# Kernel tuning notes

Hardware: AMD Instinct MI355X
Metric: run time of the kernel (lower is better)

Reference implementation:

```python
import jax, jax.numpy as jnp
import numpy as np

B, S, D = 2, 11253, 256
NHEAD, NLEVEL, DFF = 8, 4, 1024
KERNEL = 2
NPOINT = KERNEL * KERNEL
HEAD_DIM = D // NHEAD
LEVEL_SHAPES = [(92, 92), (46, 46), (23, 23), (12, 12)]
LEVEL_STARTS = np.cumsum([0] + [h * w for h, w in LEVEL_SHAPES])[:-1]


def _kernel_indices():
    # BoxeR _create_kernel_indices: even kernel -> [-0.5, 0.5]/K, (x, y) order
    idx = np.arange(KERNEL, dtype=np.float32) - (KERNEL - 1) / 2.0
    i, j = np.meshgrid(idx, idx, indexing="ij")
    return jnp.asarray(np.stack([j, i], -1).reshape(-1, 2) / KERNEL)


KIDX = _kernel_indices()  # (NPOINT, 2) box-relative sample offsets


def layer_norm(x, w, b, eps=1e-5):
    mu = x.mean(-1, keepdims=True)
    var = ((x - mu) ** 2).mean(-1, keepdims=True)
    return (x - mu) * jax.lax.rsqrt(var + eps) * w + b


def setup_inputs() -> dict:
    key = jax.random.key(0)
    ks = jax.random.split(key, 12)

    def p(i, shape, scale=0.02):
        return jax.random.normal(ks[i], shape, jnp.float32) * scale

    cxcy = jax.random.uniform(ks[2], (B, S, 2), jnp.float32, minval=0.1, maxval=0.9)
    wh = jax.random.uniform(ks[3], (B, S, 2), jnp.float32, minval=0.02, maxval=0.2)
    return dict(
        src=jax.random.normal(ks[0], (B, S, D), jnp.float32),
        pos=jax.random.normal(ks[1], (B, S, D), jnp.float32),
        src_shape=jnp.asarray(np.array(LEVEL_SHAPES, np.int32)),
        src_mask=jnp.zeros((B, S), jnp.bool_),
        src_start_index=jnp.asarray(LEVEL_STARTS.astype(np.int32)),
        src_valid_ratios=jnp.ones((B, NLEVEL, 2), jnp.float32),
        ref_windows=jnp.concatenate([cxcy, wh], -1),
        value_w=p(4, (D, D)), value_b=jnp.zeros((D,), jnp.float32),
        out_w=p(5, (D, D)), out_b=jnp.zeros((D,), jnp.float32),
        box_w=p(6, (NHEAD * NLEVEL * 4, D)), box_b=jnp.zeros((NHEAD * NLEVEL * 4,), jnp.float32),
        attn_w=p(7, (NHEAD * NLEVEL * NPOINT, D)), attn_b=jnp.zeros((NHEAD * NLEVEL * NPOINT,), jnp.float32),
        lin1_w=p(8, (DFF, D)), lin1_b=jnp.zeros((DFF,), jnp.float32),
        lin2_w=p(9, (D, DFF)), lin2_b=jnp.zeros((D,), jnp.float32),
        norm1_w=jnp.ones((D,), jnp.float32), norm1_b=jnp.zeros((D,), jnp.float32),
        norm2_w=jnp.ones((D,), jnp.float32), norm2_b=jnp.zeros((D,), jnp.float32),
    )


def box_attention(q, src, src_mask, src_valid_ratios, ref_windows,
                  value_w, value_b, out_w, out_b, box_w, box_b, attn_w, attn_b):
    value = src @ value_w.T + value_b
    value = jnp.where(src_mask[..., None], 0.0, value)
    value = value.reshape(B, S, NHEAD, HEAD_DIM)

    # where-to-attend: per-head, per-level box offsets decoded around ref_windows (cx,cy,w,h)
    off = (q @ box_w.T + box_b).reshape(B, S, NHEAD, NLEVEL, 4)
    ref = ref_windows[:, :, None, None, :]
    boxes = ref + off / 8.0 * ref[..., jnp.array([2, 3, 2, 3])]
    center, size = boxes[..., None, :2], boxes[..., None, 2:]
    grid = center + KIDX * jax.nn.relu(size)  # (B,S,nh,L,P,2) in normalized [0,1] coords
    grid = grid * src_valid_ratios[:, None, None, :, None, :]

    attn = (q @ attn_w.T + attn_b).reshape(B, S, NHEAD, NLEVEL * NPOINT)
    attn = jax.nn.softmax(attn, -1).reshape(B, S, NHEAD, NLEVEL, NPOINT)

    out = jnp.zeros((B, NHEAD, S, HEAD_DIM), src.dtype)
    for lvl, (H, W) in enumerate(LEVEL_SHAPES):
        s0 = int(LEVEL_STARTS[lvl])
        v = jnp.transpose(value[:, s0:s0 + H * W], (0, 2, 1, 3))  # (B,nh,HW,hd)
        loc = jnp.transpose(grid[:, :, :, lvl], (0, 2, 1, 3, 4))  # (B,nh,S,P,2)
        # grid_sample bilinear, align_corners=False, zero padding
        px = loc[..., 0] * W - 0.5
        py = loc[..., 1] * H - 0.5
        x0, y0 = jnp.floor(px), jnp.floor(py)
        wx, wy = (px - x0)[..., None], (py - y0)[..., None]

        def gather(ix, iy):
            valid = (ix >= 0) & (ix < W) & (iy >= 0) & (iy < H)
            idx = (jnp.clip(iy, 0, H - 1) * W + jnp.clip(ix, 0, W - 1)).astype(jnp.int32)
            g = jnp.take_along_axis(v, idx.reshape(B, NHEAD, S * NPOINT)[..., None], axis=2)
            return g.reshape(B, NHEAD, S, NPOINT, HEAD_DIM) * valid[..., None]

        g00, g01 = gather(x0, y0), gather(x0 + 1, y0)
        g10, g11 = gather(x0, y0 + 1), gather(x0 + 1, y0 + 1)
        samp = (g00 * (1 - wx) + g01 * wx) * (1 - wy) + (g10 * (1 - wx) + g11 * wx) * wy
        aw = jnp.transpose(attn[:, :, :, lvl], (0, 2, 1, 3))  # (B,nh,S,P)
        out = out + jnp.einsum("bhspd,bhsp->bhsd", samp, aw)

    out = jnp.transpose(out, (0, 2, 1, 3)).reshape(B, S, D)
    return out @ out_w.T + out_b


def reference(src, pos, src_shape, src_mask, src_start_index, src_valid_ratios,
              ref_windows, value_w, value_b, out_w, out_b, box_w, box_b,
              attn_w, attn_b, lin1_w, lin1_b, lin2_w, lin2_b,
              norm1_w, norm1_b, norm2_w, norm2_b):
    # self-attn (box attention) + residual + LN
    src2 = box_attention(src + pos, src, src_mask, src_valid_ratios, ref_windows,
                         value_w, value_b, out_w, out_b, box_w, box_b, attn_w, attn_b)
    x = layer_norm(src + src2, norm1_w, norm1_b)
    # FFN + residual + LN (dropout=0 in eval)
    ff = jax.nn.relu(x @ lin1_w.T + lin1_b) @ lin2_w.T + lin2_b
    return layer_norm(x + ff, norm2_w, norm2_b)
```

## Files before the change

kernel.cpp:

```cpp
#include <hip/hip_runtime.h>
#include <hip/hip_bf16.h>
#include <hip/hip_fp16.h>

#define TOKENS 22506
#define SLEN   11253

typedef __bf16 bf16x8 __attribute__((ext_vector_type(8)));
typedef float  f32x4  __attribute__((ext_vector_type(4)));
typedef float  f32x2  __attribute__((ext_vector_type(2)));
typedef uint   u32x4  __attribute__((ext_vector_type(4)));
typedef uint   u32x2  __attribute__((ext_vector_type(2)));

#if defined(__has_builtin)
#if __has_builtin(__builtin_amdgcn_cvt_pk_f32_fp8) && __has_builtin(__builtin_amdgcn_cvt_pk_fp8_f32)
#define HAS_FP8CVT 1
#endif
#endif

__device__ __forceinline__ ushort f2bu(float f) {
    __hip_bfloat16 h = __float2bfloat16(f);
    return *reinterpret_cast<ushort*>(&h);
}
__device__ __forceinline__ float bu2f(ushort u) {
    return __uint_as_float((uint)u << 16);
}
__device__ __forceinline__ uint pkf16(float a, float b) {
    __half2 h = __floats2half2_rn(a, b);
    return *reinterpret_cast<uint*>(&h);
}
__device__ __forceinline__ void gl16(const void* g, void* l) {
    __builtin_amdgcn_global_load_lds(
        (__attribute__((address_space(1))) void*)(g),
        (__attribute__((address_space(3))) void*)(l), 16, 0, 0);
}

#ifndef HAS_FP8CVT
__device__ __forceinline__ uint enc_fp8(float x) {
    if (!(fabsf(x) >= 0.f)) return 0;
    uint u = __float_as_uint(x);
    uint s = (u >> 24) & 0x80u;
    float ax = fabsf(x);
    if (ax >= 448.f) return s | 0x7Eu;
    if (ax < 0.0009765625f) return s;
    int e; frexpf(ax, &e);
    int ue = e - 1;
    if (ue < -6) {
        int m = (int)(ax * 512.f + 0.5f);
        if (m > 7) m = 7;
        return s | (uint)m;
    }
    float q = ax * exp2f((float)(3 - ue));
    int mi = (int)(q + 0.5f);
    if (mi >= 16) { mi >>= 1; ++ue; if (ue > 8) return s | 0x7Eu; }
    return s | ((uint)(ue + 7) << 3) | ((uint)mi & 7u);
}
__device__ __forceinline__ float dec_fp8(uint b) {
    const float sgn = (b & 0x80u) ? -1.f : 1.f;
    const uint e = (b >> 3) & 15u, m = b & 7u;
    if (e == 0) return sgn * (float)m * 0.001953125f;
    return sgn * (1.0f + (float)m * 0.125f) * exp2f((float)e - 7.f);
}
#endif

__device__ __forceinline__ uint fp8pack4(float f0, float f1, float f2, float f3) {
#ifdef HAS_FP8CVT
    int p = 0;
    p = __builtin_amdgcn_cvt_pk_fp8_f32(f0, f1, p, false);
    p = __builtin_amdgcn_cvt_pk_fp8_f32(f2, f3, p, true);
    return (uint)p;
#else
    return enc_fp8(f0) | (enc_fp8(f1) << 8) | (enc_fp8(f2) << 16) | (enc_fp8(f3) << 24);
#endif
}
__device__ __forceinline__ uint fp8pack1(float f) {
#ifdef HAS_FP8CVT
    return (uint)__builtin_amdgcn_cvt_pk_fp8_f32(f, f, 0, false) & 0xFFu;
#else
    return enc_fp8(f);
#endif
}
template<bool HI>
__device__ __forceinline__ f32x2 fp8pair(uint w) {
#ifdef HAS_FP8CVT
    auto c = __builtin_amdgcn_cvt_pk_f32_fp8((int)w, HI);
    f32x2 r; r.x = c[0]; r.y = c[1]; return r;
#else
    const uint sh = HI ? 16u : 0u;
    f32x2 r; r.x = dec_fp8((w >> sh) & 0xFFu); r.y = dec_fp8((w >> (sh + 8)) & 0xFFu);
    return r;
#endif
}

__device__ __forceinline__ void xcd_swz(int& bx, int& by) {
    const int nx = gridDim.x, ny = gridDim.y;
    if ((nx & 7) == 0) {
        const int L = blockIdx.x + nx * blockIdx.y;
        const int chunk = nx >> 3;
        const int k = L & 7, j = L >> 3;
        bx = k * chunk + (j % chunk);
        by = j / chunk;
        if (by >= ny) { bx = blockIdx.x; by = blockIdx.y; }
    } else {
        bx = blockIdx.x; by = blockIdx.y;
    }
}

template<bool RELU, bool NTSTORE, bool F8Z0>
__global__ __launch_bounds__(256) void gemm_small(
    const ushort* __restrict__ A0, const ushort* __restrict__ W0,
    const float* __restrict__ b0, void* __restrict__ C0,
    const ushort* __restrict__ A1, const ushort* __restrict__ W1,
    const float* __restrict__ b1, void* __restrict__ C1,
    int M, int N, int K)
{
    const bool zz = blockIdx.z != 0;
    const ushort* A   = zz ? A1 : A0;
    const ushort* W   = zz ? W1 : W0;
    const float* bias = zz ? b1 : b0;
    void* Cptr        = zz ? C1 : C0;

    __shared__ ushort smem[12288];
    const int tid  = threadIdx.x;
    const int lane = tid & 63;
    const int wid  = tid >> 6;
    const int wr = wid >> 1, wc = wid & 1;
    int bx, by; xcd_swz(bx, by);
    const int m0 = bx * 64, n0 = by * 128;
    const int lrow = lane & 15, lhi = lane >> 4;

    const int arow = tid >> 2;
    const int scol = (tid & 3) << 3;
    const ushort* ga  = A + (size_t)min(m0 + arow, M - 1) * K + scol;
    const ushort* gb0 = W + (size_t)(n0 + arow)      * K + scol;
    const ushort* gb1 = W + (size_t)(n0 + arow + 64) * K + scol;

    f32x4 acc[2][4] = {};
    const int NT = K >> 5;

    gl16(ga,  &smem[tid * 8]);
    gl16(gb0, &smem[4096 + tid * 8]);
    gl16(gb1, &smem[4096 + tid * 8 + 2048]);

    int cur = 0;
    for (int t = 0; t < NT; ++t) {
        __syncthreads();
        if (t + 1 < NT) {
            const int k0 = (t + 1) << 5;
            const int nb = cur ^ 1;
            gl16(ga  + k0, &smem[nb * 2048 + tid * 8]);
            gl16(gb0 + k0, &smem[4096 + nb * 4096 + tid * 8]);
            gl16(gb1 + k0, &smem[4096 + nb * 4096 + tid * 8 + 2048]);
        }
        bf16x8 afr[2], bfr[4];
        #pragma unroll
        for (int m = 0; m < 2; ++m)
            afr[m] = *reinterpret_cast<const bf16x8*>(
                &smem[cur * 2048 + (wr * 32 + m * 16 + lrow) * 32 + lhi * 8]);
        #pragma unroll
        for (int n = 0; n < 4; ++n)
            bfr[n] = *reinterpret_cast<const bf16x8*>(
                &smem[4096 + cur * 4096 + (wc * 64 + n * 16 + lrow) * 32 + lhi * 8]);
        #pragma unroll
        for (int m = 0; m < 2; ++m)
            #pragma unroll
            for (int n = 0; n < 4; ++n)
                acc[m][n] = __builtin_amdgcn_mfma_f32_16x16x32_bf16(
                    afr[m], bfr[n], acc[m][n], 0, 0, 0);
        cur ^= 1;
    }

    __syncthreads();
    #pragma unroll
    for (int m = 0; m < 2; ++m) {
        #pragma unroll
        for (int n = 0; n < 4; ++n) {
            const int col = wc * 64 + n * 16 + lrow;
            const float bv = bias[n0 + col];
            #pragma unroll
            for (int r = 0; r < 4; ++r) {
                const int row = wr * 32 + m * 16 + lhi * 4 + r;
                float v = acc[m][n][r] + bv;
                if (RELU) v = fmaxf(v, 0.f);
                smem[row * 136 + col] = f2bu(v);
            }
        }
    }
    __syncthreads();
    if (F8Z0 && !zz) {
        #pragma unroll
        for (int i = 0; i < 4; ++i) {
            const int e = tid + i * 256;
            const int row = e >> 4, ch = e & 15;
            if (m0 + row < M) {
                const u32x4 v = *reinterpret_cast<const u32x4*>(&smem[row * 136 + ch * 8]);
                float f[8];
                #pragma unroll
                for (int j = 0; j < 4; ++j) {
                    f[2 * j]     = __uint_as_float(v[j] << 16);
                    f[2 * j + 1] = __uint_as_float(v[j] & 0xFFFF0000u);
                }
                u32x2 o;
                o[0] = fp8pack4(f[0], f[1], f[2], f[3]);
                o[1] = fp8pack4(f[4], f[5], f[6], f[7]);
                u32x2* dst = reinterpret_cast<u32x2*>(
                    (unsigned char*)Cptr + (size_t)(m0 + row) * N + n0 + ch * 8);
                if (NTSTORE) __builtin_nontemporal_store(o, dst);
                else *dst = o;
            }
        }
    } else {
        #pragma unroll
        for (int i = 0; i < 4; ++i) {
            const int e = tid + i * 256;
            const int row = e >> 4, ch = e & 15;
            if (m0 + row < M) {
                const u32x4 v = *reinterpret_cast<const u32x4*>(&smem[row * 136 + ch * 8]);
                u32x4* dst = reinterpret_cast<u32x4*>(
                    (ushort*)Cptr + (size_t)(m0 + row) * N + n0 + ch * 8);
                if (NTSTORE) __builtin_nontemporal_store(v, dst);
                else *dst = v;
            }
        }
    }
}

__global__ __launch_bounds__(256) void gemm_f8(
    const unsigned char* __restrict__ A, const unsigned char* __restrict__ W,
    const float* __restrict__ bias, ushort* __restrict__ C,
    int M, int N, int K)
{
    __shared__ unsigned char smem[17408];
    const int tid  = threadIdx.x;
    const int lane = tid & 63;
    const int wid  = tid >> 6;
    const int wr = wid >> 1, wc = wid & 1;
    int bx, by; xcd_swz(bx, by);
    const int m0 = bx * 64, n0 = by * 128;
    const int lrow = lane & 15, lhi = lane >> 4;

    const int arow = tid >> 1;
    const int achk = (tid & 1) << 4;
    const unsigned char* ga = A + (size_t)min(m0 + (arow & 63), M - 1) * K + achk;
    const unsigned char* gb = W + (size_t)(n0 + arow) * K + achk;

    f32x4 acc[2][4] = {};
    const int NT = K >> 5;

    if (tid < 128) gl16(ga, &smem[tid * 16]);
    gl16(gb, &smem[4096 + tid * 16]);

    int cur = 0;
    for (int t = 0; t < NT; ++t) {
        __syncthreads();
        if (t + 1 < NT) {
            const int k0 = (t + 1) << 5;
            const int nb = cur ^ 1;
            if (tid < 128) gl16(ga + k0, &smem[nb * 2048 + tid * 16]);
            gl16(gb + k0, &smem[4096 + nb * 4096 + tid * 16]);
        }
        long afr[2], bfr[4];
        #pragma unroll
        for (int m = 0; m < 2; ++m)
            afr[m] = *reinterpret_cast<const long*>(
                &smem[cur * 2048 + (wr * 32 + m * 16 + lrow) * 32 + lhi * 8]);
        #pragma unroll
        for (int n = 0; n < 4; ++n)
            bfr[n] = *reinterpret_cast<const long*>(
                &smem[4096 + cur * 4096 + (wc * 64 + n * 16 + lrow) * 32 + lhi * 8]);
        #pragma unroll
        for (int m = 0; m < 2; ++m)
            #pragma unroll
            for (int n = 0; n < 4; ++n)
                acc[m][n] = __builtin_amdgcn_mfma_f32_16x16x32_fp8_fp8(
                    afr[m], bfr[n], acc[m][n], 0, 0, 0);
        cur ^= 1;
    }

    __syncthreads();
    ushort* sm16 = reinterpret_cast<ushort*>(smem);
    #pragma unroll
    for (int m = 0; m < 2; ++m) {
        #pragma unroll
        for (int n = 0; n < 4; ++n) {
            const int col = wc * 64 + n * 16 + lrow;
            const float bv = bias[n0 + col];
            #pragma unroll
            for (int r = 0; r < 4; ++r) {
                const int row = wr * 32 + m * 16 + lhi * 4 + r;
                sm16[row * 136 + col] = f2bu(acc[m][n][r] + bv);
            }
        }
    }
    __syncthreads();
    #pragma unroll
    for (int i = 0; i < 4; ++i) {
        const int e = tid + i * 256;
        const int row = e >> 4, ch = e & 15;
        if (m0 + row < M) {
            const u32x4 v = *reinterpret_cast<const u32x4*>(&sm16[row * 136 + ch * 8]);
            *reinterpret_cast<u32x4*>(C + (size_t)(m0 + row) * N + n0 + ch * 8) = v;
        }
    }
}

__global__ __launch_bounds__(256) void prep_all(
    const float* __restrict__ vw, const float* __restrict__ bw,
    const float* __restrict__ aw, const float* __restrict__ ow,
    const float* __restrict__ l1, const float* __restrict__ l2,
    const float* __restrict__ bb, const float* __restrict__ ab,
    ushort* __restrict__ dstW, float* __restrict__ dstQB,
    unsigned char* __restrict__ dstW8,
    const float4* __restrict__ src, const float4* __restrict__ pos,
    ushort4* __restrict__ srcb, ushort4* __restrict__ qb)
{
    const int blk = blockIdx.x;
    if (blk < 2817) {
        const int i = blk * 256 + threadIdx.x;
        if (i < 720896) {
            float v;
            if      (i <  65536) v = vw[i];
            else if (i <  98304) v = bw[i -  65536];
            else if (i < 131072) v = aw[i -  98304];
            else if (i < 196608) v = ow[i - 131072];
            else if (i < 458752) v = l1[i - 196608];
            else                 v = l2[i - 458752];
            dstW[i] = f2bu(v);
            if (i >= 458752) dstW8[i - 458752] = (unsigned char)fp8pack1(v);
        } else if (i < 721152) {
            const int j = i - 720896;
            dstQB[j] = (j < 128) ? bb[j] : ab[j - 128];
        }
    } else {
        const int i = (blk - 2817) * 256 + threadIdx.x;
        if (i >= TOKENS * 64) return;
        const float4 s = src[i], p = pos[i];
        ushort4 us, uq;
        us.x = f2bu(s.x); us.y = f2bu(s.y); us.z = f2bu(s.z); us.w = f2bu(s.w);
        uq.x = f2bu(s.x + p.x); uq.y = f2bu(s.y + p.y);
        uq.z = f2bu(s.z + p.z); uq.w = f2bu(s.w + p.w);
        srcb[i] = us; qb[i] = uq;
    }
}

__global__ __launch_bounds__(256) void box_fused(
    const unsigned char* __restrict__ val,
    const ushort* __restrict__ qout,
    const float* __restrict__ refw,
    const float* __restrict__ vratio,
    ushort* __restrict__ attnout)
{
    __shared__ ushort4 offs[64 * 17];
    __shared__ uint2 wts[64 * 17];
    const int tid = threadIdx.x;

    int work;
    {
        const int x = blockIdx.x & 7, s = blockIdx.x >> 3;
        work = (x < 4) ? (s * 4 + x) : (1408 + s * 4 + (x - 4));
        if ((int)gridDim.x != 2814 || work >= (int)gridDim.x) work = blockIdx.x;
    }
    const int t0 = work * 8;

    {
        const int u = tid >> 2, lvl = tid & 3;
        const int t = min(t0 + (u >> 3), TOKENS - 1);
        const int h = u & 7;
        const int b = (t >= SLEN) ? 1 : 0;
        const ushort* qr = qout + (size_t)t * 256;

        const uint2 lu = *reinterpret_cast<const uint2*>(qr + 128 + h * 16 + lvl * 4);
        float e0 = __uint_as_float(lu.x << 16);
        float e1 = __uint_as_float(lu.x & 0xFFFF0000u);
        float e2 = __uint_as_float(lu.y << 16);
        float e3 = __uint_as_float(lu.y & 0xFFFF0000u);
        float mx = fmaxf(fmaxf(e0, e1), fmaxf(e2, e3));
        mx = fmaxf(mx, __shfl_xor(mx, 1));
        mx = fmaxf(mx, __shfl_xor(mx, 2));
        e0 = __expf(e0 - mx); e1 = __expf(e1 - mx);
        e2 = __expf(e2 - mx); e3 = __expf(e3 - mx);
        float ss = e0 + e1 + e2 + e3;
        ss += __shfl_xor(ss, 1);
        ss += __shfl_xor(ss, 2);
        const float inv = 1.f / ss;
        const float pe[4] = { e0 * inv, e1 * inv, e2 * inv, e3 * inv };

        const uint2 ou = *reinterpret_cast<const uint2*>(qr + h * 16 + lvl * 4);
        const float o0 = __uint_as_float(ou.x << 16) * 0.125f;
        const float o1 = __uint_as_float(ou.x & 0xFFFF0000u) * 0.125f;
        const float o2 = __uint_as_float(ou.y << 16) * 0.125f;
        const float o3 = __uint_as_float(ou.y & 0xFFFF0000u) * 0.125f;

        const float4 rw = *reinterpret_cast<const float4*>(refw + (size_t)t * 4);
        const int Ww = (lvl == 0) ? 92 : (lvl == 1) ? 46 : (lvl == 2) ? 23 : 12;
        const int s0 = (lvl == 0) ? 0 : (lvl == 1) ? 8464 : (lvl == 2) ? 10580 : 11109;
        const float vrx = vratio[(b * 4 + lvl) * 2 + 0];
        const float vry = vratio[(b * 4 + lvl) * 2 + 1];

        const float bx  = rw.x + o0 * rw.z;
        const float by  = rw.y + o1 * rw.w;
        const float bwd = fmaxf(rw.z + o2 * rw.z, 0.f);
        const float bhd = fmaxf(rw.w + o3 * rw.w, 0.f);

        #pragma unroll
        for (int k = 0; k < 4; ++k) {
            const float jx = (k & 1) ? 0.25f : -0.25f;
            const float iy = (k & 2) ? 0.25f : -0.25f;
            const float px = (bx + jx * bwd) * vrx * (float)Ww - 0.5f;
            const float py = (by + iy * bhd) * vry * (float)Ww - 0.5f;
            const float x0f = floorf(px), y0f = floorf(py);
            const int x0 = (int)x0f, y0 = (int)y0f;
            const float wx = px - x0f, wy = py - y0f;
            const float wp = pe[k];

            const bool vx0 = (x0 >= 0) && (x0 < Ww);
            const bool vx1 = (x0 + 1 >= 0) && (x0 + 1 < Ww);
            const bool vy0 = (y0 >= 0) && (y0 < Ww);
            const bool vy1 = (y0 + 1 >= 0) && (y0 + 1 < Ww);
            const int cx0 = min(max(x0, 0), Ww - 1);
            const int cx1 = min(max(x0 + 1, 0), Ww - 1);
            const int cy0 = min(max(y0, 0), Ww - 1);
            const int cy1 = min(max(y0 + 1, 0), Ww - 1);

            const float w00 = (vx0 && vy0) ? wp * (1.f - wx) * (1.f - wy) : 0.f;
            const float w01 = (vx1 && vy0) ? wp * wx         * (1.f - wy) : 0.f;
            const float w10 = (vx0 && vy1) ? wp * (1.f - wx) * wy         : 0.f;
            const float w11 = (vx1 && vy1) ? wp * wx         * wy         : 0.f;

            ushort4 sp;
            sp.x = (ushort)(s0 + cy0 * Ww + cx0);
            sp.y = (ushort)(s0 + cy0 * Ww + cx1);
            sp.z = (ushort)(s0 + cy1 * Ww + cx0);
            sp.w = (ushort)(s0 + cy1 * Ww + cx1);

            const int p = lvl * 4 + k;
            offs[u * 17 + p] = sp;
            wts[u * 17 + p]  = make_uint2(pkf16(w00, w01), pkf16(w10, w11));
        }
    }
    __syncthreads();

    const int u = tid >> 2, dl = tid & 3;
    const int traw = t0 + (u >> 3);
    const int t = min(traw, TOKENS - 1);
    const int h = u & 7;
    const uint boff = ((t >= SLEN) ? (uint)SLEN * 256u : 0u) + (uint)h * 32u + (uint)dl * 8u;
    const char* base = (const char*)val;

    const ushort4* po = &offs[u * 17];
    const uint2* pw = &wts[u * 17];
    f32x2 a0 = {0.f, 0.f}, a1 = {0.f, 0.f}, a2 = {0.f, 0.f}, a3 = {0.f, 0.f};

    uint2 vA[16], vB[16];

    auto issue = [&](int g, uint2 (&v)[16]) {
        #pragma unroll
        for (int q = 0; q < 4; ++q) {
            const ushort4 sp = po[g * 4 + q];
            v[q * 4 + 0] = *reinterpret_cast<const uint2*>(base + (((uint)sp.x << 8) + boff));
            v[q * 4 + 1] = *reinterpret_cast<const uint2*>(base + (((uint)sp.y << 8) + boff));
            v[q * 4 + 2] = *reinterpret_cast<const uint2*>(base + (((uint)sp.z << 8) + boff));
            v[q * 4 + 3] = *reinterpret_cast<const uint2*>(base + (((uint)sp.w << 8) + boff));
        }
    };
    auto consume = [&](int g, uint2 (&v)[16]) {
        #pragma unroll
        for (int q = 0; q < 4; ++q) {
            const uint2 w2 = pw[g * 4 + q];
            const float2 wl = __half22float2(*reinterpret_cast<const __half2*>(&w2.x));
            const float2 wh = __half22float2(*reinterpret_cast<const __half2*>(&w2.y));
            const float wq[4] = { wl.x, wl.y, wh.x, wh.y };
            #pragma unroll
            for (int c = 0; c < 4; ++c) {
                const uint2 vv = v[q * 4 + c];
                f32x2 wv; wv.x = wq[c]; wv.y = wq[c];
                a0 += wv * fp8pair<false>(vv.x);
                a1 += wv * fp8pair<true>(vv.x);
                a2 += wv * fp8pair<false>(vv.y);
                a3 += wv * fp8pair<true>(vv.y);
            }
        }
    };

    issue(0, vA);
    issue(1, vB);
    __builtin_amdgcn_sched_barrier(0);
    consume(0, vA);
    issue(2, vA);
    __builtin_amdgcn_sched_barrier(0);
    consume(1, vB);
    issue(3, vB);
    __builtin_amdgcn_sched_barrier(0);
    consume(2, vA);
    consume(3, vB);

    if (traw < TOKENS) {
        u32x4 o;
        o[0] = (uint)f2bu(a0.x) | ((uint)f2bu(a0.y) << 16);
        o[1] = (uint)f2bu(a1.x) | ((uint)f2bu(a1.y) << 16);
        o[2] = (uint)f2bu(a2.x) | ((uint)f2bu(a2.y) << 16);
        o[3] = (uint)f2bu(a3.x) | ((uint)f2bu(a3.y) << 16);
        *reinterpret_cast<u32x4*>(attnout + (size_t)t * 256 + h * 32 + dl * 8) = o;
    }
}

template<bool AF32, bool OUTF32>
__global__ __launch_bounds__(256) void ln_add2(
    const void* __restrict__ aptr, const ushort* __restrict__ bptr,
    const float* __restrict__ w, const float* __restrict__ bias,
    void* __restrict__ outp, int nrows)
{
    const int lane = threadIdx.x & 63, wv = threadIdx.x >> 6;
    const int row = blockIdx.x * 4 + wv;
    if (row >= nrows) return;
    const size_t base = (size_t)row * 256 + lane * 4;

    float4 av;
    if (AF32) {
        av = *reinterpret_cast<const float4*>((const float*)aptr + base);
    } else {
        const ushort4 u = *reinterpret_cast<const ushort4*>((const ushort*)aptr + base);
        av = make_float4(bu2f(u.x), bu2f(u.y), bu2f(u.z), bu2f(u.w));
    }
    const ushort4 ub = *reinterpret_cast<const ushort4*>(bptr + base);
    const float v0 = av.x + bu2f(ub.x), v1 = av.y + bu2f(ub.y);
    const float v2 = av.z + bu2f(ub.z), v3 = av.w + bu2f(ub.w);

    float s = v0 + v1 + v2 + v3;
    #pragma unroll
    for (int o = 32; o; o >>= 1) s += __shfl_xor(s, o);
    const float mu = s * (1.f / 256.f);
    const float d0 = v0 - mu, d1 = v1 - mu, d2 = v2 - mu, d3 = v3 - mu;
    float s2 = d0 * d0 + d1 * d1 + d2 * d2 + d3 * d3;
    #pragma unroll
    for (int o = 32; o; o >>= 1) s2 += __shfl_xor(s2, o);
    const float rs = rsqrtf(s2 * (1.f / 256.f) + 1e-5f);

    const float4 w4 = *reinterpret_cast<const float4*>(w + lane * 4);
    const float4 g4 = *reinterpret_cast<const float4*>(bias + lane * 4);
    const float r0 = d0 * rs * w4.x + g4.x;
    const float r1 = d1 * rs * w4.y + g4.y;
    const float r2 = d2 * rs * w4.z + g4.z;
    const float r3 = d3 * rs * w4.w + g4.w;
    if (OUTF32) {
        *reinterpret_cast<float4*>((float*)outp + base) = make_float4(r0, r1, r2, r3);
    } else {
        ushort4 u;
        u.x = f2bu(r0); u.y = f2bu(r1); u.z = f2bu(r2); u.w = f2bu(r3);
        *reinterpret_cast<ushort4*>((ushort*)outp + base) = u;
    }
}

extern "C" void kernel_launch(void* const* d_in, const int* in_sizes, int n_in,
                              void* d_out, int out_size, void* d_ws, size_t ws_size,
                              hipStream_t stream)
{
    const float* src     = (const float*)d_in[0];
    const float* pos     = (const float*)d_in[1];
    const float* vratio  = (const float*)d_in[5];
    const float* refw    = (const float*)d_in[6];
    const float* value_w = (const float*)d_in[7];
    const float* value_b = (const float*)d_in[8];
    const float* out_w   = (const float*)d_in[9];
    const float* out_b   = (const float*)d_in[10];
    const float* box_w   = (const float*)d_in[11];
    const float* box_b   = (const float*)d_in[12];
    const float* attn_w  = (const float*)d_in[13];
    const float* attn_b  = (const float*)d_in[14];
    const float* lin1_w  = (const float*)d_in[15];
    const float* lin1_b  = (const float*)d_in[16];
    const float* lin2_w  = (const float*)d_in[17];
    const float* lin2_b  = (const float*)d_in[18];
    const float* n1w     = (const float*)d_in[19];
    const float* n1b     = (const float*)d_in[20];
    const float* n2w     = (const float*)d_in[21];
    const float* n2b     = (const float*)d_in[22];

    char* wsb = (char*)d_ws;
    ushort* Wb    = (ushort*)(wsb);
    float*  qcb   = (float*)(wsb + 1441792);
    ushort* srcb  = (ushort*)(wsb + 1442816);
    ushort* qb    = (ushort*)(wsb + 12965888);
    unsigned char* valb = (unsigned char*)(wsb + 24488960);
    ushort* qoutb = (ushort*)(wsb + 36012032);
    ushort* attb  = (ushort*)(wsb + 47535104);
    ushort* src2b = (ushort*)(wsb + 59058176);
    ushort* xbb   = (ushort*)(wsb + 70581248);
    unsigned char* hb8 = (unsigned char*)(wsb + 82104320);
    ushort* yb    = (ushort*)(wsb + 105150464);
    unsigned char* Wf8 = (unsigned char*)(wsb + 116673536);

    const dim3 blk(256);

    prep_all<<<dim3(8444), blk, 0, stream>>>(
        value_w, box_w, attn_w, out_w, lin1_w, lin2_w, box_b, attn_b, Wb, qcb,
        Wf8, (const float4*)src, (const float4*)pos, (ushort4*)srcb, (ushort4*)qb);

    gemm_small<false, false, true><<<dim3(352, 2, 2), blk, 0, stream>>>(
        srcb, Wb, value_b, valb,
        qb, Wb + 65536, qcb, qoutb, TOKENS, 256, 256);

    box_fused<<<dim3((TOKENS + 7) / 8), blk, 0, stream>>>(
        valb, qoutb, refw, vratio, attb);

    gemm_small<false, false, false><<<dim3(352, 2, 1), blk, 0, stream>>>(
        attb, Wb + 131072, out_b, src2b,
        attb, Wb + 131072, out_b, src2b, TOKENS, 256, 256);
    ln_add2<false, false><<<dim3((TOKENS + 3) / 4), blk, 0, stream>>>(
        srcb, src2b, n1w, n1b, xbb, TOKENS);
    gemm_small<true, true, true><<<dim3(352, 8, 1), blk, 0, stream>>>(
        xbb, Wb + 196608, lin1_b, hb8,
        xbb, Wb + 196608, lin1_b, hb8, TOKENS, 1024, 256);
    gemm_f8<<<dim3(352, 2), blk, 0, stream>>>(
        hb8, Wf8, lin2_b, yb, TOKENS, 256, 1024);
    ln_add2<false, true><<<dim3((TOKENS + 3) / 4), blk, 0, stream>>>(
        xbb, yb, n2w, n2b, (float*)d_out, TOKENS);
}
```

Before: 131.0 us.

## Split bilinear corners across lane pairs with 16-byte gathers and shuffle reduction

Changes the thread-to-work mapping in the deformable sampling kernel. Each lane now loads 16 fp8 channels per corner with 128-bit loads, covering only two of the four bilinear corners, instead of 8 channels for all four corners. The partial sums from the two corner groups are combined with an xor-shuffle before writing bf16 output. This halves the number of gather instructions in exchange for wider loads, more accumulator registers, and extra shuffles. It also drops the explicit double-buffered issue/consume schedule.

```diff
diff --git a/kernel.cpp b/kernel.cpp
--- a/kernel.cpp
+++ b/kernel.cpp
@@ -440,66 +440,79 @@
     __syncthreads();
 
     const int u = tid >> 2, dl = tid & 3;
+    const int hd = dl & 1;
+    const int cp = dl >> 1;
     const int traw = t0 + (u >> 3);
     const int t = min(traw, TOKENS - 1);
     const int h = u & 7;
-    const uint boff = ((t >= SLEN) ? (uint)SLEN * 256u : 0u) + (uint)h * 32u + (uint)dl * 8u;
+    const uint boff = ((t >= SLEN) ? (uint)SLEN * 256u : 0u)
+                    + (uint)h * 32u + (uint)hd * 16u;
     const char* base = (const char*)val;
 
     const ushort4* po = &offs[u * 17];
     const uint2* pw = &wts[u * 17];
-    f32x2 a0 = {0.f, 0.f}, a1 = {0.f, 0.f}, a2 = {0.f, 0.f}, a3 = {0.f, 0.f};
-
-    uint2 vA[16], vB[16];
-
-    auto issue = [&](int g, uint2 (&v)[16]) {
-        #pragma unroll
-        for (int q = 0; q < 4; ++q) {
-            const ushort4 sp = po[g * 4 + q];
-            v[q * 4 + 0] = *reinterpret_cast<const uint2*>(base + (((uint)sp.x << 8) + boff));
-            v[q * 4 + 1] = *reinterpret_cast<const uint2*>(base + (((uint)sp.y << 8) + boff));
-            v[q * 4 + 2] = *reinterpret_cast<const uint2*>(base + (((uint)sp.z << 8) + boff));
-            v[q * 4 + 3] = *reinterpret_cast<const uint2*>(base + (((uint)sp.w << 8) + boff));
-        }
+    f32x2 ac0 = {0,0}, ac1 = {0,0}, ac2 = {0,0}, ac3 = {0,0};
+    f32x2 ac4 = {0,0}, ac5 = {0,0}, ac6 = {0,0}, ac7 = {0,0};
+
+    #pragma unroll
+    for (int g = 0; g < 8; ++g) {
+        const ushort4 spA = po[g * 2 + 0];
+        const ushort4 spB = po[g * 2 + 1];
+        const uint2  wA  = pw[g * 2 + 0];
+        const uint2  wB  = pw[g * 2 + 1];
+
+        const uint rA0 = cp ? (uint)spA.z : (uint)spA.x;
+        const uint rA1 = cp ? (uint)spA.w : (uint)spA.y;
+        const uint rB0 = cp ? (uint)spB.z : (uint)spB.x;
+        const uint rB1 = cp ? (uint)spB.w : (uint)spB.y;
+
+        const u32x4 vA0 = *reinterpret_cast<const u32x4*>(base + ((rA0 << 8) + boff));
+        const u32x4 vA1 = *reinterpret_cast<const u32x4*>(base + ((rA1 << 8) + boff));
+        const u32x4 vB0 = *reinterpret_cast<const u32x4*>(base + ((rB0 << 8) + boff));
+        const u32x4 vB1 = *reinterpret_cast<const u32x4*>(base + ((rB1 << 8) + boff));
+
+        const uint wAu = cp ? wA.y : wA.x;
+        const uint wBu = cp ? wB.y : wB.x;
+        const float2 wAf = __half22float2(*reinterpret_cast<const __half2*>(&wAu));
+        const float2 wBf = __half22float2(*reinterpret_cast<const __half2*>(&wBu));
+
+        auto acc16 = [&](const u32x4 v, const float w) {
+            f32x2 wv; wv.x = w; wv.y = w;
+            ac0 += wv * fp8pair<false>(v[0]);
+            ac1 += wv * fp8pair<true >(v[0]);
+            ac2 += wv * fp8pair<false>(v[1]);
+            ac3 += wv * fp8pair<true >(v[1]);
+            ac4 += wv * fp8pair<false>(v[2]);
+            ac5 += wv * fp8pair<true >(v[2]);
+            ac6 += wv * fp8pair<false>(v[3]);
+            ac7 += wv * fp8pair<true >(v[3]);
+        };
+        acc16(vA0, wAf.x); acc16(vA1, wAf.y);
+        acc16(vB0, wBf.x); acc16(vB1, wBf.y);
+    }
+
+    auto xsum = [&](f32x2& a) {
+        a.x += __shfl_xor(a.x, 2);
+        a.y += __shfl_xor(a.y, 2);
     };
-    auto consume = [&](int g, uint2 (&v)[16]) {
-        #pragma unroll
-        for (int q = 0; q < 4; ++q) {
-            const uint2 w2 = pw[g * 4 + q];
-            const float2 wl = __half22float2(*reinterpret_cast<const __half2*>(&w2.x));
-            const float2 wh = __half22float2(*reinterpret_cast<const __half2*>(&w2.y));
-            const float wq[4] = { wl.x, wl.y, wh.x, wh.y };
-            #pragma unroll
-            for (int c = 0; c < 4; ++c) {
-                const uint2 vv = v[q * 4 + c];
-                f32x2 wv; wv.x = wq[c]; wv.y = wq[c];
-                a0 += wv * fp8pair<false>(vv.x);
-                a1 += wv * fp8pair<true>(vv.x);
-                a2 += wv * fp8pair<false>(vv.y);
-                a3 += wv * fp8pair<true>(vv.y);
-            }
-        }
-    };
-
-    issue(0, vA);
-    issue(1, vB);
-    __builtin_amdgcn_sched_barrier(0);
-    consume(0, vA);
-    issue(2, vA);
-    __builtin_amdgcn_sched_barrier(0);
-    consume(1, vB);
-    issue(3, vB);
-    __builtin_amdgcn_sched_barrier(0);
-    consume(2, vA);
-    consume(3, vB);
+    xsum(ac0); xsum(ac1); xsum(ac2); xsum(ac3);
+    xsum(ac4); xsum(ac5); xsum(ac6); xsum(ac7);
 
     if (traw < TOKENS) {
         u32x4 o;
-        o[0] = (uint)f2bu(a0.x) | ((uint)f2bu(a0.y) << 16);
-        o[1] = (uint)f2bu(a1.x) | ((uint)f2bu(a1.y) << 16);
-        o[2] = (uint)f2bu(a2.x) | ((uint)f2bu(a2.y) << 16);
-        o[3] = (uint)f2bu(a3.x) | ((uint)f2bu(a3.y) << 16);
-        *reinterpret_cast<u32x4*>(attnout + (size_t)t * 256 + h * 32 + dl * 8) = o;
+        if (cp == 0) {
+            o[0] = (uint)f2bu(ac0.x) | ((uint)f2bu(ac0.y) << 16);
+            o[1] = (uint)f2bu(ac1.x) | ((uint)f2bu(ac1.y) << 16);
+            o[2] = (uint)f2bu(ac2.x) | ((uint)f2bu(ac2.y) << 16);
+            o[3] = (uint)f2bu(ac3.x) | ((uint)f2bu(ac3.y) << 16);
+        } else {
+            o[0] = (uint)f2bu(ac4.x) | ((uint)f2bu(ac4.y) << 16);
+            o[1] = (uint)f2bu(ac5.x) | ((uint)f2bu(ac5.y) << 16);
+            o[2] = (uint)f2bu(ac6.x) | ((uint)f2bu(ac6.y) << 16);
+            o[3] = (uint)f2bu(ac7.x) | ((uint)f2bu(ac7.y) << 16);
+        }
+        *reinterpret_cast<u32x4*>(
+            attnout + (size_t)t * 256 + h * 32 + hd * 16 + cp * 8) = o;
     }
 }
 
```

New measurement: 130.4 us (median of 2 runs). About the same (-0.5%).
